# Kernel tuning notes

Measured on AMD Instinct MI355X. Metric: run time of the kernel, lower is better.

Reference implementation:

```python
import jax, jax.numpy as jnp
import numpy as np

D_MODEL = 512
NUM_HEADS = 8
DEPTH = D_MODEL // NUM_HEADS


def setup_inputs() -> dict:
    key = jax.random.key(0)
    kx, kq, kk, kv, ko = jax.random.split(key, 5)
    B, S = 2, 4096
    X = jax.random.normal(kx, (B, S, D_MODEL), dtype=jnp.float32)
    # Dense(use_bias=False) kernels: [in, out]
    scale = 1.0 / np.sqrt(D_MODEL)
    Wq = jax.random.normal(kq, (D_MODEL, D_MODEL), dtype=jnp.float32) * scale
    Wk = jax.random.normal(kk, (D_MODEL, D_MODEL), dtype=jnp.float32) * scale
    Wv = jax.random.normal(kv, (D_MODEL, D_MODEL), dtype=jnp.float32) * scale
    Wo = jax.random.normal(ko, (D_MODEL, D_MODEL), dtype=jnp.float32) * scale
    return {"X": X, "Wq": Wq, "Wk": Wk, "Wv": Wv, "Wo": Wo}


def reference(X, Wq, Wk, Wv, Wo):
    B, S, _ = X.shape
    H, Dh = NUM_HEADS, DEPTH

    def split_heads(t):  # [B,S,D] -> [B,H,S,Dh]
        return t.reshape(B, S, H, Dh).transpose(0, 2, 1, 3)

    Qh = split_heads(X @ Wq)
    Kh = split_heads(X @ Wk)
    Vh = split_heads(X @ Wv)

    inv_scale = 1.0 / jnp.sqrt(jnp.float32(Dh))
    scores = jnp.einsum('bhqd,bhkd->bhqk', Qh, Kh) * inv_scale
    attn = jax.nn.softmax(scores, axis=-1)
    context = jnp.einsum('bhqk,bhkd->bhqd', attn, Vh)
    combined = context.transpose(0, 2, 1, 3).reshape(B, S, H * Dh)
    return combined @ Wo
```

## Files before the change

kernel.cpp:

```cpp
#include <hip/hip_runtime.h>

#define D_MODEL 512
#define NHEADS 8
#define DH 64
#define BATCH 2
#define SEQ 4096
#define MTOT (BATCH*SEQ)

typedef __attribute__((ext_vector_type(8))) short bf16x8;
typedef __attribute__((ext_vector_type(4))) short s16x4;
typedef __attribute__((ext_vector_type(4))) float f32x4;
typedef __attribute__((ext_vector_type(16))) float f32x16;

__device__ __forceinline__ unsigned short f2b(float f) {
  unsigned int u = __float_as_uint(f);
  u = (u + 0x7fffu + ((u >> 16) & 1u)) >> 16;
  return (unsigned short)u;
}

__device__ __forceinline__ float fexp2(float x) {
  return __builtin_amdgcn_exp2f(x);
}

__device__ __forceinline__ unsigned int cvtpk_bf16(float a, float b) {
  unsigned int r;
  asm("v_cvt_pk_bf16_f32 %0, %1, %2" : "=v"(r) : "v"(a), "v"(b));
  return r;
}

__device__ __forceinline__ void tr16(unsigned addr, s16x4& d) {
  asm volatile("ds_read_b64_tr_b16 %0, %1" : "=v"(d) : "v"(addr));
}


__global__ void cvt_x_kernel(const float* __restrict__ X,
                             unsigned short* __restrict__ Xb, int n) {
  int i = (blockIdx.x * blockDim.x + threadIdx.x) * 8;
  if (i >= n) return;
  const float4* s = (const float4*)(X + i);
  float4 v0 = s[0], v1 = s[1];
  union { bf16x8 v; unsigned short u[8]; } r;
  r.u[0] = f2b(v0.x); r.u[1] = f2b(v0.y); r.u[2] = f2b(v0.z); r.u[3] = f2b(v0.w);
  r.u[4] = f2b(v1.x); r.u[5] = f2b(v1.y); r.u[6] = f2b(v1.z); r.u[7] = f2b(v1.w);
  *(bf16x8*)(Xb + i) = r.v;
}

__global__ void cvt_w_kernel(const float* __restrict__ W0, const float* __restrict__ W1,
                             const float* __restrict__ W2, const float* __restrict__ W3,
                             unsigned short* __restrict__ Wt) {
  const float* Ws[4] = {W0, W1, W2, W3};
  const float* W = Ws[blockIdx.y];
  int t = blockIdx.x * blockDim.x + threadIdx.x;
  int k = t >> 9, n = t & 511;
  Wt[(size_t)blockIdx.y * (512*512) + (size_t)n * 512 + k] = f2b(W[t]);
}

__global__ __launch_bounds__(256) void gemm128_kernel(
    const unsigned short* __restrict__ A,
    const unsigned short* __restrict__ WtAll,
    unsigned short* __restrict__ qkv,
    float* __restrict__ outF,
    int modeParam) {
  int mode = (modeParam < 0) ? (int)blockIdx.z : modeParam;
  const unsigned short* Wt = WtAll + (size_t)((modeParam < 0) ? blockIdx.z : 0) * (512*512);

  __shared__ __align__(16) unsigned short Alds[128][72];
  __shared__ __align__(16) unsigned short Blds[128][72];

  int t = threadIdx.x;
  int lane = t & 63, wave = t >> 6;
  int wr = wave >> 1, wc = wave & 1;
  int lr = lane & 15, lg = lane >> 4;
  int mBase = blockIdx.x * 128;
  int nBase = blockIdx.y * 128;

  f32x4 zero = {0.f, 0.f, 0.f, 0.f};
  f32x4 acc[4][4];
#pragma unroll
  for (int i = 0; i < 4; i++)
#pragma unroll
    for (int j = 0; j < 4; j++) acc[i][j] = zero;

  int seg = t & 7, r0 = t >> 3;

  for (int k0 = 0; k0 < 512; k0 += 64) {
#pragma unroll
    for (int p = 0; p < 4; ++p) {
      int row = r0 + p * 32;
      *(int4*)&Alds[row][seg * 8] =
          *(const int4*)(A + (size_t)(mBase + row) * 512 + k0 + seg * 8);
      *(int4*)&Blds[row][seg * 8] =
          *(const int4*)(Wt + (size_t)(nBase + row) * 512 + k0 + seg * 8);
    }
    __syncthreads();
#pragma unroll
    for (int kk = 0; kk < 64; kk += 32) {
      bf16x8 afr[4], bfr[4];
#pragma unroll
      for (int mi = 0; mi < 4; mi++)
        afr[mi] = *(const bf16x8*)&Alds[wr * 64 + mi * 16 + lr][kk + lg * 8];
#pragma unroll
      for (int ni = 0; ni < 4; ni++)
        bfr[ni] = *(const bf16x8*)&Blds[wc * 64 + ni * 16 + lr][kk + lg * 8];
#pragma unroll
      for (int mi = 0; mi < 4; mi++)
#pragma unroll
        for (int ni = 0; ni < 4; ni++)
          acc[mi][ni] = __builtin_amdgcn_mfma_f32_16x16x32_bf16(
              afr[mi], bfr[ni], acc[mi][ni], 0, 0, 0);
    }
    __syncthreads();
  }

#pragma unroll
  for (int mi = 0; mi < 4; mi++) {
#pragma unroll
    for (int ni = 0; ni < 4; ni++) {
#pragma unroll
      for (int rg = 0; rg < 4; rg++) {
        int r = mBase + wr * 64 + mi * 16 + lg * 4 + rg;
        int c = nBase + wc * 64 + ni * 16 + lr;
        float v = acc[mi][ni][rg];
        if (mode < 3) {
          int b = r >> 12, s = r & 4095, h = c >> 6, d = c & 63;
          qkv[(size_t)mode * ((size_t)MTOT * 512) +
              ((((size_t)b * NHEADS + h) * SEQ + s) * DH + d)] = f2b(v);
        } else {
          outF[(size_t)r * 512 + c] = v;
        }
      }
    }
  }
}

__global__ __launch_bounds__(256) void attn_kernel(
    const unsigned short* __restrict__ Qb,
    const unsigned short* __restrict__ Kb,
    const unsigned short* __restrict__ Vb,
    unsigned short* __restrict__ CTX) {
  int flat = blockIdx.x;
  int xcd = flat & 7, jj = flat >> 3;
  int bh = xcd + ((jj >> 5) << 3);
  int qc = jj & 31;
  int b = bh >> 3, h = bh & 7;
  const unsigned short* Qp = Qb + (size_t)bh * SEQ * DH;
  const unsigned short* Kp = Kb + (size_t)bh * SEQ * DH;
  const unsigned short* Vp = Vb + (size_t)bh * SEQ * DH;

  __shared__ __align__(128) unsigned short Kl[2][64][72];
  __shared__ __align__(128) unsigned short Vl[2][4096];
  __shared__ __align__(128) unsigned short PT[4][32][72];

  int t = threadIdx.x;
  int lane = t & 63, wave = t >> 6;
  int q = lane & 31, hv = lane >> 5;
  int lr = lane & 15, lg2 = (lane >> 4) & 1;
  int q0w = qc * 128 + wave * 32;

  bf16x8 aq[4];
#pragma unroll
  for (int s = 0; s < 4; s++)
    aq[s] = *(const bf16x8*)(Qp + (size_t)(q0w + q) * DH + s * 16 + hv * 8);

  f32x16 o0, o1;
#pragma unroll
  for (int i = 0; i < 16; i++) { o0[i] = 0.f; o1[i] = 0.f; }
  float m2 = -1e30f, lsum = 0.f;

  const float c2 = 0.125f * 1.44269504088896340736f;

  int srow = t >> 3, sseg = t & 7;
  const int NT = SEQ / 64;

  unsigned vtr_lane = (unsigned)(hv * 1024 + lg2 * 128 + lr * 8);
  unsigned vbuf0 = (unsigned)(size_t)&Vl[0][0];
  unsigned vbuf1 = (unsigned)(size_t)&Vl[1][0];

  int4 kreg[2], vreg[2];
#pragma unroll
  for (int p = 0; p < 2; ++p) {
    int row = srow + p * 32;
    kreg[p] = *(const int4*)(Kp + (size_t)row * DH + sseg * 8);
    vreg[p] = *(const int4*)(Vp + (size_t)row * DH + sseg * 8);
  }

  for (int kb = 0; kb < NT; ++kb) {
    int cur = kb & 1;
#pragma unroll
    for (int p = 0; p < 2; ++p) {
      int row = srow + p * 32;
      *(int4*)&Kl[cur][row][sseg * 8] = kreg[p];
      int vdst = ((row >> 2) * 4 + (sseg >> 1)) * 64 + (row & 3) * 16 + (sseg & 1) * 8;
      *(int4*)&Vl[cur][vdst] = vreg[p];
    }
    if (kb + 1 < NT) {
#pragma unroll
      for (int p = 0; p < 2; ++p) {
        int row = srow + p * 32;
        kreg[p] = *(const int4*)(Kp + (size_t)((kb + 1) * 64 + row) * DH + sseg * 8);
        vreg[p] = *(const int4*)(Vp + (size_t)((kb + 1) * 64 + row) * DH + sseg * 8);
      }
    }
    __syncthreads();

    f32x16 s0, s1;
#pragma unroll
    for (int i = 0; i < 16; i++) { s0[i] = 0.f; s1[i] = 0.f; }
    __builtin_amdgcn_s_setprio(1);
#pragma unroll
    for (int s = 0; s < 4; s++) {
      bf16x8 bk0 = *(const bf16x8*)&Kl[cur][q][s * 16 + hv * 8];
      bf16x8 bk1 = *(const bf16x8*)&Kl[cur][32 + q][s * 16 + hv * 8];
      s0 = __builtin_amdgcn_mfma_f32_32x32x16_bf16(bk0, aq[s], s0, 0, 0, 0);
      s1 = __builtin_amdgcn_mfma_f32_32x32x16_bf16(bk1, aq[s], s1, 0, 0, 0);
    }
    __builtin_amdgcn_s_setprio(0);

    float pm;
    {
      float a0 = fmaxf(fmaxf(s0[0], s0[1]), fmaxf(s0[2], s0[3]));
      float a1 = fmaxf(fmaxf(s0[4], s0[5]), fmaxf(s0[6], s0[7]));
      float a2 = fmaxf(fmaxf(s0[8], s0[9]), fmaxf(s0[10], s0[11]));
      float a3 = fmaxf(fmaxf(s0[12], s0[13]), fmaxf(s0[14], s0[15]));
      float b0 = fmaxf(fmaxf(s1[0], s1[1]), fmaxf(s1[2], s1[3]));
      float b1 = fmaxf(fmaxf(s1[4], s1[5]), fmaxf(s1[6], s1[7]));
      float b2 = fmaxf(fmaxf(s1[8], s1[9]), fmaxf(s1[10], s1[11]));
      float b3 = fmaxf(fmaxf(s1[12], s1[13]), fmaxf(s1[14], s1[15]));
      pm = fmaxf(fmaxf(fmaxf(a0, a1), fmaxf(a2, a3)),
                 fmaxf(fmaxf(b0, b1), fmaxf(b2, b3))) * c2;
    }
    pm = fmaxf(pm, __shfl_xor(pm, 32));

    if (!__all((int)(pm <= m2 + 8.f))) {
      float mn = fmaxf(m2, pm);
      float corr = fexp2(m2 - mn);
      m2 = mn;
      lsum *= corr;
#pragma unroll
      for (int i = 0; i < 16; i++) { o0[i] *= corr; o1[i] *= corr; }
    }

    float rs = 0.f;
#pragma unroll
    for (int rg = 0; rg < 4; rg++) {
      float p0 = fexp2(fmaf(s0[rg * 4 + 0], c2, -m2));
      float p1 = fexp2(fmaf(s0[rg * 4 + 1], c2, -m2));
      float p2 = fexp2(fmaf(s0[rg * 4 + 2], c2, -m2));
      float p3 = fexp2(fmaf(s0[rg * 4 + 3], c2, -m2));
      rs += (p0 + p1) + (p2 + p3);
      uint2 w; w.x = cvtpk_bf16(p0, p1); w.y = cvtpk_bf16(p2, p3);
      *(uint2*)&PT[wave][q][rg * 8 + hv * 4] = w;
      float q0_ = fexp2(fmaf(s1[rg * 4 + 0], c2, -m2));
      float q1_ = fexp2(fmaf(s1[rg * 4 + 1], c2, -m2));
      float q2_ = fexp2(fmaf(s1[rg * 4 + 2], c2, -m2));
      float q3_ = fexp2(fmaf(s1[rg * 4 + 3], c2, -m2));
      rs += (q0_ + q1_) + (q2_ + q3_);
      uint2 w2; w2.x = cvtpk_bf16(q0_, q1_); w2.y = cvtpk_bf16(q2_, q3_);
      *(uint2*)&PT[wave][q][32 + rg * 8 + hv * 4] = w2;
    }
    rs += __shfl_xor(rs, 32);
    lsum += rs;

    bf16x8 ap[4];
#pragma unroll
    for (int s = 0; s < 4; s++)
      ap[s] = *(const bf16x8*)&PT[wave][q][s * 16 + hv * 8];

    unsigned vb = (cur ? vbuf1 : vbuf0) + vtr_lane;
    {
      union { bf16x8 v; s16x4 hh[2]; } bv[4];
#pragma unroll
      for (int s = 0; s < 4; s++) {
        tr16(vb + s * 2048 + 0 * 512 + 0 * 256, bv[s].hh[0]);
        tr16(vb + s * 2048 + 1 * 512 + 0 * 256, bv[s].hh[1]);
      }
      asm volatile("s_waitcnt lgkmcnt(0)" ::: "memory");
      __builtin_amdgcn_sched_barrier(0);
      __builtin_amdgcn_s_setprio(1);
#pragma unroll
      for (int s = 0; s < 4; s++)
        o0 = __builtin_amdgcn_mfma_f32_32x32x16_bf16(bv[s].v, ap[s], o0, 0, 0, 0);
      __builtin_amdgcn_s_setprio(0);
    }
    {
      union { bf16x8 v; s16x4 hh[2]; } bv[4];
#pragma unroll
      for (int s = 0; s < 4; s++) {
        tr16(vb + s * 2048 + 0 * 512 + 1 * 256, bv[s].hh[0]);
        tr16(vb + s * 2048 + 1 * 512 + 1 * 256, bv[s].hh[1]);
      }
      asm volatile("s_waitcnt lgkmcnt(0)" ::: "memory");
      __builtin_amdgcn_sched_barrier(0);
      __builtin_amdgcn_s_setprio(1);
#pragma unroll
      for (int s = 0; s < 4; s++)
        o1 = __builtin_amdgcn_mfma_f32_32x32x16_bf16(bv[s].v, ap[s], o1, 0, 0, 0);
      __builtin_amdgcn_s_setprio(0);
    }
  }

  float inv = 1.f / lsum;
#pragma unroll
  for (int rg = 0; rg < 4; rg++) {
    uint2 w;
    w.x = cvtpk_bf16(o0[rg * 4 + 0] * inv, o0[rg * 4 + 1] * inv);
    w.y = cvtpk_bf16(o0[rg * 4 + 2] * inv, o0[rg * 4 + 3] * inv);
    *(uint2*)&PT[wave][q][rg * 8 + hv * 4] = w;
    uint2 w2;
    w2.x = cvtpk_bf16(o1[rg * 4 + 0] * inv, o1[rg * 4 + 1] * inv);
    w2.y = cvtpk_bf16(o1[rg * 4 + 2] * inv, o1[rg * 4 + 3] * inv);
    *(uint2*)&PT[wave][q][32 + rg * 8 + hv * 4] = w2;
  }

  int qr = lane >> 1, half = lane & 1;
  size_t base = ((size_t)(b * SEQ + q0w + qr)) * 512 + h * 64 + half * 32;
#pragma unroll
  for (int i = 0; i < 4; i++) {
    bf16x8 w = *(const bf16x8*)&PT[wave][qr][half * 32 + i * 8];
    *(bf16x8*)(CTX + base + i * 8) = w;
  }
}


extern "C" void kernel_launch(void* const* d_in, const int* in_sizes, int n_in,
                              void* d_out, int out_size, void* d_ws, size_t ws_size,
                              hipStream_t stream) {
  const float* X  = (const float*)d_in[0];
  const float* Wq = (const float*)d_in[1];
  const float* Wk = (const float*)d_in[2];
  const float* Wv = (const float*)d_in[3];
  const float* Wo = (const float*)d_in[4];
  float* out = (float*)d_out;

  char* ws = (char*)d_ws;
  unsigned short* Wqt = (unsigned short*)(ws);
  unsigned short* Wot = (unsigned short*)(ws + 3u * 524288u);
  unsigned short* Xb  = (unsigned short*)(ws + 4u * 524288u);
  unsigned short* Qb  = (unsigned short*)(ws + 4u * 524288u + 8388608u);
  unsigned short* Kb  = Qb + (size_t)MTOT * 512;
  unsigned short* Vb  = Kb + (size_t)MTOT * 512;
  unsigned short* CTX = Vb + (size_t)MTOT * 512;

  int nX = MTOT * D_MODEL;
  cvt_x_kernel<<<dim3(nX / (8 * 256)), dim3(256), 0, stream>>>(X, Xb, nX);
  cvt_w_kernel<<<dim3(1024, 4), dim3(256), 0, stream>>>(Wq, Wk, Wv, Wo, Wqt);
  gemm128_kernel<<<dim3(64, 4, 3), dim3(256), 0, stream>>>(Xb, Wqt, Qb, nullptr, -1);
  attn_kernel<<<dim3(512), dim3(256), 0, stream>>>(Qb, Kb, Vb, CTX);
  gemm128_kernel<<<dim3(64, 4, 1), dim3(256), 0, stream>>>(CTX, Wot, nullptr, out, 3);
}
```

Measured before the change: 212.4 us.

## Split attention KV loop across two wave groups with split-K softmax merge

```diff
diff --git a/kernel.cpp b/kernel.cpp
--- a/kernel.cpp
+++ b/kernel.cpp
@@ -133,7 +133,7 @@
   }
 }
 
-__global__ __launch_bounds__(256) void attn_kernel(
+__global__ __launch_bounds__(512) void attn_kernel(
     const unsigned short* __restrict__ Qb,
     const unsigned short* __restrict__ Kb,
     const unsigned short* __restrict__ Vb,
@@ -149,13 +149,14 @@
 
   __shared__ __align__(128) unsigned short Kl[2][64][72];
   __shared__ __align__(128) unsigned short Vl[2][4096];
-  __shared__ __align__(128) unsigned short PT[4][32][72];
+  __shared__ __align__(128) unsigned short PT[8][32][72];
 
   int t = threadIdx.x;
   int lane = t & 63, wave = t >> 6;
+  int lw = wave & 3, grp = wave >> 2;
   int q = lane & 31, hv = lane >> 5;
   int lr = lane & 15, lg2 = (lane >> 4) & 1;
-  int q0w = qc * 128 + wave * 32;
+  int q0w = qc * 128 + lw * 32;
 
   bf16x8 aq[4];
 #pragma unroll
@@ -170,35 +171,31 @@
   const float c2 = 0.125f * 1.44269504088896340736f;
 
   int srow = t >> 3, sseg = t & 7;
-  const int NT = SEQ / 64;
+  int vdst = ((srow >> 2) * 4 + (sseg >> 1)) * 64 + (srow & 3) * 16 + (sseg & 1) * 8;
+  const int NIT = SEQ / 128;
 
   unsigned vtr_lane = (unsigned)(hv * 1024 + lg2 * 128 + lr * 8);
-  unsigned vbuf0 = (unsigned)(size_t)&Vl[0][0];
-  unsigned vbuf1 = (unsigned)(size_t)&Vl[1][0];
+  unsigned vbuf = (unsigned)(size_t)&Vl[grp][0] + vtr_lane;
 
   int4 kreg[2], vreg[2];
 #pragma unroll
   for (int p = 0; p < 2; ++p) {
-    int row = srow + p * 32;
-    kreg[p] = *(const int4*)(Kp + (size_t)row * DH + sseg * 8);
-    vreg[p] = *(const int4*)(Vp + (size_t)row * DH + sseg * 8);
-  }
-
-  for (int kb = 0; kb < NT; ++kb) {
-    int cur = kb & 1;
+    kreg[p] = *(const int4*)(Kp + (size_t)(p * 64 + srow) * DH + sseg * 8);
+    vreg[p] = *(const int4*)(Vp + (size_t)(p * 64 + srow) * DH + sseg * 8);
+  }
+
+  for (int it = 0; it < NIT; ++it) {
 #pragma unroll
     for (int p = 0; p < 2; ++p) {
-      int row = srow + p * 32;
-      *(int4*)&Kl[cur][row][sseg * 8] = kreg[p];
-      int vdst = ((row >> 2) * 4 + (sseg >> 1)) * 64 + (row & 3) * 16 + (sseg & 1) * 8;
-      *(int4*)&Vl[cur][vdst] = vreg[p];
-    }
-    if (kb + 1 < NT) {
+      *(int4*)&Kl[p][srow][sseg * 8] = kreg[p];
+      *(int4*)&Vl[p][vdst] = vreg[p];
+    }
+    if (it + 1 < NIT) {
 #pragma unroll
       for (int p = 0; p < 2; ++p) {
-        int row = srow + p * 32;
-        kreg[p] = *(const int4*)(Kp + (size_t)((kb + 1) * 64 + row) * DH + sseg * 8);
-        vreg[p] = *(const int4*)(Vp + (size_t)((kb + 1) * 64 + row) * DH + sseg * 8);
+        int rowg = (it + 1) * 128 + p * 64 + srow;
+        kreg[p] = *(const int4*)(Kp + (size_t)rowg * DH + sseg * 8);
+        vreg[p] = *(const int4*)(Vp + (size_t)rowg * DH + sseg * 8);
       }
     }
     __syncthreads();
@@ -209,8 +206,8 @@
     __builtin_amdgcn_s_setprio(1);
 #pragma unroll
     for (int s = 0; s < 4; s++) {
-      bf16x8 bk0 = *(const bf16x8*)&Kl[cur][q][s * 16 + hv * 8];
-      bf16x8 bk1 = *(const bf16x8*)&Kl[cur][32 + q][s * 16 + hv * 8];
+      bf16x8 bk0 = *(const bf16x8*)&Kl[grp][q][s * 16 + hv * 8];
+      bf16x8 bk1 = *(const bf16x8*)&Kl[grp][32 + q][s * 16 + hv * 8];
       s0 = __builtin_amdgcn_mfma_f32_32x32x16_bf16(bk0, aq[s], s0, 0, 0, 0);
       s1 = __builtin_amdgcn_mfma_f32_32x32x16_bf16(bk1, aq[s], s1, 0, 0, 0);
     }
@@ -266,13 +263,12 @@
     for (int s = 0; s < 4; s++)
       ap[s] = *(const bf16x8*)&PT[wave][q][s * 16 + hv * 8];
 
-    unsigned vb = (cur ? vbuf1 : vbuf0) + vtr_lane;
     {
       union { bf16x8 v; s16x4 hh[2]; } bv[4];
 #pragma unroll
       for (int s = 0; s < 4; s++) {
-        tr16(vb + s * 2048 + 0 * 512 + 0 * 256, bv[s].hh[0]);
-        tr16(vb + s * 2048 + 1 * 512 + 0 * 256, bv[s].hh[1]);
+        tr16(vbuf + s * 2048 + 0 * 512 + 0 * 256, bv[s].hh[0]);
+        tr16(vbuf + s * 2048 + 1 * 512 + 0 * 256, bv[s].hh[1]);
       }
       asm volatile("s_waitcnt lgkmcnt(0)" ::: "memory");
       __builtin_amdgcn_sched_barrier(0);
@@ -286,8 +282,8 @@
       union { bf16x8 v; s16x4 hh[2]; } bv[4];
 #pragma unroll
       for (int s = 0; s < 4; s++) {
-        tr16(vb + s * 2048 + 0 * 512 + 1 * 256, bv[s].hh[0]);
-        tr16(vb + s * 2048 + 1 * 512 + 1 * 256, bv[s].hh[1]);
+        tr16(vbuf + s * 2048 + 0 * 512 + 1 * 256, bv[s].hh[0]);
+        tr16(vbuf + s * 2048 + 1 * 512 + 1 * 256, bv[s].hh[1]);
       }
       asm volatile("s_waitcnt lgkmcnt(0)" ::: "memory");
       __builtin_amdgcn_sched_barrier(0);
@@ -297,27 +293,53 @@
         o1 = __builtin_amdgcn_mfma_f32_32x32x16_bf16(bv[s].v, ap[s], o1, 0, 0, 0);
       __builtin_amdgcn_s_setprio(0);
     }
-  }
-
-  float inv = 1.f / lsum;
-#pragma unroll
-  for (int rg = 0; rg < 4; rg++) {
-    uint2 w;
-    w.x = cvtpk_bf16(o0[rg * 4 + 0] * inv, o0[rg * 4 + 1] * inv);
-    w.y = cvtpk_bf16(o0[rg * 4 + 2] * inv, o0[rg * 4 + 3] * inv);
-    *(uint2*)&PT[wave][q][rg * 8 + hv * 4] = w;
-    uint2 w2;
-    w2.x = cvtpk_bf16(o1[rg * 4 + 0] * inv, o1[rg * 4 + 1] * inv);
-    w2.y = cvtpk_bf16(o1[rg * 4 + 2] * inv, o1[rg * 4 + 3] * inv);
-    *(uint2*)&PT[wave][q][32 + rg * 8 + hv * 4] = w2;
-  }
-
-  int qr = lane >> 1, half = lane & 1;
-  size_t base = ((size_t)(b * SEQ + q0w + qr)) * 512 + h * 64 + half * 32;
-#pragma unroll
-  for (int i = 0; i < 4; i++) {
-    bf16x8 w = *(const bf16x8*)&PT[wave][qr][half * 32 + i * 8];
-    *(bf16x8*)(CTX + base + i * 8) = w;
+    __syncthreads();
+  }
+
+  float* mf = (float*)&PT[wave][0][0];
+  if (hv == 0) { mf[q] = m2; mf[32 + q] = lsum; }
+  __syncthreads();
+  float* pmf = (float*)&PT[wave ^ 4][0][0];
+  float pm_ = pmf[q], pl_ = pmf[32 + q];
+  float mm = fmaxf(m2, pm_);
+  float sc = fexp2(m2 - mm);
+  float psc = fexp2(pm_ - mm);
+  float ltot = lsum * sc + pl_ * psc;
+
+  float* scr = (lw < 2) ? ((float*)&Kl[0][0][0] + lw * 2048)
+                        : ((float*)&Vl[0][0] + (lw - 2) * 2048);
+  if (grp == 1) {
+#pragma unroll
+    for (int i = 0; i < 16; i++) scr[i * 64 + lane] = o0[i] * sc;
+#pragma unroll
+    for (int i = 0; i < 16; i++) scr[(16 + i) * 64 + lane] = o1[i] * sc;
+  }
+  __syncthreads();
+  if (grp == 0) {
+    float inv = 1.f / ltot;
+#pragma unroll
+    for (int i = 0; i < 16; i++) o0[i] = (o0[i] * sc + scr[i * 64 + lane]) * inv;
+#pragma unroll
+    for (int i = 0; i < 16; i++) o1[i] = (o1[i] * sc + scr[(16 + i) * 64 + lane]) * inv;
+
+#pragma unroll
+    for (int rg = 0; rg < 4; rg++) {
+      uint2 w;
+      w.x = cvtpk_bf16(o0[rg * 4 + 0], o0[rg * 4 + 1]);
+      w.y = cvtpk_bf16(o0[rg * 4 + 2], o0[rg * 4 + 3]);
+      *(uint2*)&PT[wave][q][rg * 8 + hv * 4] = w;
+      uint2 w2;
+      w2.x = cvtpk_bf16(o1[rg * 4 + 0], o1[rg * 4 + 1]);
+      w2.y = cvtpk_bf16(o1[rg * 4 + 2], o1[rg * 4 + 3]);
+      *(uint2*)&PT[wave][q][32 + rg * 8 + hv * 4] = w2;
+    }
+    int qr = lane >> 1, half = lane & 1;
+    size_t base = ((size_t)(b * SEQ + q0w + qr)) * 512 + h * 64 + half * 32;
+#pragma unroll
+    for (int i = 0; i < 4; i++) {
+      bf16x8 w = *(const bf16x8*)&PT[wave][qr][half * 32 + i * 8];
+      *(bf16x8*)(CTX + base + i * 8) = w;
+    }
   }
 }
 
@@ -345,6 +367,6 @@
   cvt_x_kernel<<<dim3(nX / (8 * 256)), dim3(256), 0, stream>>>(X, Xb, nX);
   cvt_w_kernel<<<dim3(1024, 4), dim3(256), 0, stream>>>(Wq, Wk, Wv, Wo, Wqt);
   gemm128_kernel<<<dim3(64, 4, 3), dim3(256), 0, stream>>>(Xb, Wqt, Qb, nullptr, -1);
-  attn_kernel<<<dim3(512), dim3(256), 0, stream>>>(Qb, Kb, Vb, CTX);
+  attn_kernel<<<dim3(512), dim3(512), 0, stream>>>(Qb, Kb, Vb, CTX);
   gemm128_kernel<<<dim3(64, 4, 1), dim3(256), 0, stream>>>(CTX, Wot, nullptr, out, 3);
 }
```

Result: slower. 267.4 us (+25.9%).
